# Performance work log

Measured on AMD Instinct MI355X. Metric: run time of the kernel, lower is better.

## Reference

```python
import jax, jax.numpy as jnp
import numpy as np


def setup_inputs() -> dict:
    key = jax.random.key(0)
    ks = jax.random.split(key, 8)
    T, B, D = 2048, 8, 1024
    d, NM, k = 64, 8, 2
    Mp1 = NM + 1
    s_in = 1.0 / np.sqrt(D)
    X = jax.random.normal(ks[0], (T, B, D), dtype=jnp.float32)
    M0 = 0.02 * jax.random.normal(ks[1], (d, d), dtype=jnp.float32)
    W_q = s_in * jax.random.normal(ks[2], (D, d), dtype=jnp.float32)
    b_q = jnp.zeros((d,), jnp.float32)
    W_k = s_in * jax.random.normal(ks[3], (D, Mp1 * d), dtype=jnp.float32)
    b_k = jnp.zeros((Mp1 * d,), jnp.float32)
    W_v = s_in * jax.random.normal(ks[4], (D, Mp1 * d), dtype=jnp.float32)
    b_v = jnp.zeros((Mp1 * d,), jnp.float32)
    W_g = s_in * jax.random.normal(ks[5], (D, NM), dtype=jnp.float32)
    b_g = jnp.zeros((NM,), jnp.float32)
    return dict(X=X, M0=M0, W_q=W_q, b_q=b_q, W_k=W_k, b_k=b_k,
                W_v=W_v, b_v=b_v, W_g=W_g, b_g=b_g, k=k)


def _mom_forward(X, M0, W_q, b_q, W_k, b_k, W_v, b_v, W_g, b_g, k):
    T, B, D = X.shape
    d = M0.shape[0]
    NM = W_g.shape[1]
    Mp1 = NM + 1  # memory 0 is the always-on shared memory
    Kp1 = k + 1
    # --- gating + top-k memory selection ---
    scores = jax.nn.softmax(X @ W_g + b_g, axis=-1)               # (T,B,NM)
    m_sc, m_idx = jax.lax.top_k(scores, k)                        # (T,B,k)
    m_sc = m_sc / jnp.sum(m_sc, axis=-1, keepdims=True)
    m_idx = m_idx + 1                                             # shift: 0 reserved for shared memory
    idx_u = jnp.concatenate([jnp.zeros((T, B, 1), m_idx.dtype), m_idx], axis=2)  # (T,B,Kp1)
    sc_u = jnp.concatenate([jnp.ones((T, B, 1), m_sc.dtype), m_sc], axis=2)      # (T,B,Kp1)
    # --- varlen pack: sort replicated tokens by (batch, memory, time) ---
    # NB: the torch build_varlen_pack runs under @torch.no_grad -> detached
    t_rep = jnp.broadcast_to(jnp.arange(T)[:, None, None], (T, B, Kp1)).reshape(-1)
    b_rep = jnp.broadcast_to(jnp.arange(B)[None, :, None], (T, B, Kp1)).reshape(-1)
    m_rep = idx_u.reshape(-1)
    sort_key = b_rep * (Mp1 * T) + m_rep * T + t_rep              # unique per packed token
    perm = jnp.argsort(sort_key)
    t_o = t_rep[perm]
    b_o = b_rep[perm]
    m_id = m_rep[perm]
    alpha = jax.lax.stop_gradient(sc_u.reshape(-1)[perm])         # (Tt,)
    x_tilde = jax.lax.stop_gradient(
        jnp.broadcast_to(X[:, :, None, :], (T, B, Kp1, D)).reshape(-1, D)[perm])  # (Tt,D)
    Tt = T * B * Kp1
    # segment id per packed token; state resets at each new (batch, memory) segment
    seg = b_o * Mp1 + m_id
    new_seg = jnp.concatenate([jnp.ones((1,), bool), seg[1:] != seg[:-1]])
    # --- projections; pick k/v head matching each token's routed memory ---
    q_t = x_tilde @ W_q + b_q                                     # (Tt,d)
    K_all = (x_tilde @ W_k + b_k).reshape(Tt, Mp1, d)
    V_all = (x_tilde @ W_v + b_v).reshape(Tt, Mp1, d)
    k_t = jnp.take_along_axis(K_all, m_id[:, None, None], axis=1)[:, 0]  # (Tt,d)
    v_t = jnp.take_along_axis(V_all, m_id[:, None, None], axis=1)[:, 0]  # (Tt,d)
    # --- per-segment linear-attention recurrence: M_t = M0 + sum k_tau v_tau^T, o_t = q_t @ M_t ---
    def step(M, inp):
        qt, kt, vt, ns = inp
        M = jnp.where(ns, M0, M)
        M = M + kt[:, None] * vt[None, :]
        return M, qt @ M
    _, o_tilde = jax.lax.scan(step, M0, (q_t, k_t, v_t, new_seg))  # (Tt,d)
    # --- weighted scatter-add back to (T,B,d) ---
    o = jnp.zeros((T, B, d), X.dtype).at[t_o, b_o].add(alpha[:, None] * o_tilde)
    return o


def reference(X, M0, W_q, b_q, W_k, b_k, W_v, b_v, W_g, b_g, k):
    return _mom_forward(X, M0, W_q, b_q, W_k, b_k, W_v, b_v, W_g, b_g, k)
```

## Files before the change

kernel.cpp:

```cpp
#include <hip/hip_runtime.h>

#define TT   2048
#define BB   8
#define DD   1024
#define HD   64
#define MP1  9
#define NTOK (TT*BB)
#define CH   64
#define NC   32
#define NSEG (BB*MP1)
#define SEGCAP 2048
#define NCAT 1280
#define LDP  72
#define NZB  1024

typedef __attribute__((ext_vector_type(8))) short bf16x8;
typedef __attribute__((ext_vector_type(4))) float f32x4;

union U8 { uint4 v; unsigned short s[8]; };

static __device__ __forceinline__ unsigned short f2bf(float f) {
  union { float f; unsigned u; } c; c.f = f;
  unsigned r = (c.u + 0x7FFF + ((c.u >> 16) & 1)) >> 16;
  return (unsigned short)r;
}
static __device__ __forceinline__ float bf2f(unsigned short s) {
  union { unsigned u; float f; } c; c.u = ((unsigned)s) << 16;
  return c.f;
}

static __device__ __forceinline__ int sched_walk(
    const int* __restrict__ seglen, int bid, int* chunk_out) {
  const int batch = bid & 7;
  int idx = bid >> 3;
  for (int m = 0; m < MP1; m++) {
    int nch = (seglen[batch * MP1 + m] + 63) >> 6;
    if (idx < nch) { *chunk_out = idx; return batch * MP1 + m; }
    idx -= nch;
  }
  return -1;
}

__global__ __launch_bounds__(256) void prep(
    const float* __restrict__ X,
    const float* __restrict__ Wq, const float* __restrict__ Wk,
    const float* __restrict__ Wv, const float* __restrict__ bq,
    const float* __restrict__ bk, const float* __restrict__ bv,
    const float* __restrict__ Wg, const float* __restrict__ bg,
    unsigned short* __restrict__ Wt, float* __restrict__ bcat,
    int2* __restrict__ idxb, float2* __restrict__ alfb,
    unsigned short* __restrict__ Xb,
    float4* __restrict__ outz, int n4) {
  __shared__ float smem[8 * DD];
  const int tid = threadIdx.x;
  const int id = blockIdx.x;
  if (id >= 1344) {
    int i = (id - 1344) * 256 + tid;
    if (i < n4) outz[i] = make_float4(0.f, 0.f, 0.f, 0.f);
    return;
  }
  if (id < 320) {
    float (*tile)[65] = (float(*)[65])smem;
    const int n0 = (id % 20) * 64, k0 = (id / 20) * 64;
    const int c = tid & 63, rr = tid >> 6;
#pragma unroll 4
    for (int i = 0; i < 16; i++) {
      int kk = k0 + rr * 16 + i;
      int n  = n0 + c;
      float v = 0.f;
      if (n0 < 64)        v = Wq[kk * 64 + n];
      else if (n0 < 640)  v = Wk[kk * 576 + (n - 64)];
      else if (n0 < 1216) v = Wv[kk * 576 + (n - 640)];
      tile[rr * 16 + i][c] = v;
    }
    __syncthreads();
    const int lk = (tid & 15) * 4, ln = tid >> 4;
#pragma unroll
    for (int p = 0; p < 4; p++) {
      int nl = p * 16 + ln;
      ushort4 o;
      o.x = f2bf(tile[lk + 0][nl]); o.y = f2bf(tile[lk + 1][nl]);
      o.z = f2bf(tile[lk + 2][nl]); o.w = f2bf(tile[lk + 3][nl]);
      *(ushort4*)&Wt[(size_t)(n0 + nl) * DD + k0 + lk] = o;
    }
    if (id == 0) {
      for (int idx = tid; idx < NCAT; idx += 256) {
        float b = 0.f;
        if (idx < 64)        b = bq[idx];
        else if (idx < 640)  b = bk[idx - 64];
        else if (idx < 1216) b = bv[idx - 640];
        bcat[idx] = b;
      }
    }
    return;
  }
  float* wgT = smem;
#pragma unroll
  for (int idx4 = tid; idx4 < 2048; idx4 += 256) {
    float4 v = *(const float4*)&Wg[(size_t)idx4 * 4];
    int flat = idx4 * 4;
    int i = flat >> 3, j = flat & 7;
    wgT[(j + 0) * DD + i] = v.x;
    wgT[(j + 1) * DD + i] = v.y;
    wgT[(j + 2) * DD + i] = v.z;
    wgT[(j + 3) * DD + i] = v.w;
  }
  __syncthreads();
  const int lane = tid & 63, wave = tid >> 6;
  const int base_tok = (id - 320) * 16 + wave * 4;
  for (int tk = 0; tk < 4; tk++) {
    const int tok = base_tok + tk;
    const float* xr = X + (size_t)tok * DD;
    unsigned short* xbr = Xb + ((size_t)((tok & 7) * TT + (tok >> 3))) * DD;
    float p[8] = {0.f,0.f,0.f,0.f,0.f,0.f,0.f,0.f};
#pragma unroll
    for (int it = 0; it < 4; it++) {
      int i = it * 256 + lane * 4;
      float4 x = *(const float4*)&xr[i];
      ushort4 o;
      o.x = f2bf(x.x); o.y = f2bf(x.y); o.z = f2bf(x.z); o.w = f2bf(x.w);
      *(ushort4*)&xbr[i] = o;
#pragma unroll
      for (int j = 0; j < 8; j++) {
        float4 wv = *(const float4*)&wgT[j * DD + i];
        p[j] += x.x * wv.x + x.y * wv.y + x.z * wv.z + x.w * wv.w;
      }
    }
#pragma unroll
    for (int j = 0; j < 8; j++) {
      float v = p[j];
#pragma unroll
      for (int off = 32; off > 0; off >>= 1) v += __shfl_xor(v, off);
      p[j] = v + bg[j];
    }
    if (lane == 0) {
      int i1 = 0; float z1 = p[0];
#pragma unroll
      for (int j = 1; j < 8; j++) if (p[j] > z1) { z1 = p[j]; i1 = j; }
      int i2 = -1; float z2 = -3.0e38f;
#pragma unroll
      for (int j = 0; j < 8; j++) if (j != i1 && p[j] > z2) { z2 = p[j]; i2 = j; }
      float e   = expf(z2 - z1);
      float inv = 1.0f / (1.0f + e);
      idxb[tok] = make_int2(i1 + 1, i2 + 1);
      alfb[tok] = make_float2(inv, e * inv);
    }
  }
}

__global__ __launch_bounds__(1024) void pack_kernel(
    const int2* __restrict__ idxb, const float2* __restrict__ alfb,
    int* __restrict__ tlist, float* __restrict__ alist,
    int* __restrict__ seglen) {
  const int seg = blockIdx.x;
  const int b = seg / MP1, m = seg % MP1;
  const int tid = threadIdx.x;
  int* tl = tlist + (size_t)seg * SEGCAP;
  float* al = alist + (size_t)seg * SEGCAP;
  if (m == 0) {
    for (int pos = tid; pos < TT; pos += 1024) { tl[pos] = pos; al[pos] = 1.f; }
    if (tid == 0) seglen[seg] = TT;
    return;
  }
  __shared__ int wsum[16];
  const int lane = tid & 63, w = tid >> 6;
  int base = 0;
  for (int r = 0; r < TT / 1024; r++) {
    int t = r * 1024 + tid;
    int2 ix = idxb[t * BB + b];
    bool f = (ix.x == m || ix.y == m);
    float2 af = alfb[t * BB + b];
    float alpha = (ix.x == m) ? af.x : af.y;
    unsigned long long mask = __ballot(f);
    int lanepos = __popcll(mask & ((1ull << lane) - 1ull));
    if (lane == 0) wsum[w] = __popcll(mask);
    __syncthreads();
    int wbase = 0, total = 0;
#pragma unroll
    for (int i = 0; i < 16; i++) { int v = wsum[i]; if (i < w) wbase += v; total += v; }
    if (f) { int pos = base + wbase + lanepos; tl[pos] = t; al[pos] = alpha; }
    base += total;
    __syncthreads();
  }
  if (tid == 0) seglen[seg] = base;
  int Lpad = (base + 63) & ~63;
  for (int pos = base + tid; pos < Lpad; pos += 1024) { tl[pos] = 0; al[pos] = 0.f; }
}

#define ABUF_H 2048
#define BBUF_H 6144

__global__ __launch_bounds__(256) void pkv_intra(
    const unsigned short* __restrict__ Xb, const unsigned short* __restrict__ Wt,
    const float* __restrict__ bcat,
    const int* __restrict__ tlist, const float* __restrict__ alist,
    const int* __restrict__ seglen,
    unsigned short* __restrict__ Sb16, unsigned short* __restrict__ Qd,
    float* __restrict__ out) {
  int chunk;
  const int seg = sched_walk(seglen, blockIdx.x, &chunk);
  if (seg < 0) return;
  const int t0 = chunk * 64;
  const int L = seglen[seg];
  const int b = seg / MP1, m = seg % MP1;
  __shared__ unsigned short lds[4 * 64 * LDP];
  __shared__ int tls[64];
  unsigned short* Asb = lds;
  unsigned short* Bsb = lds + 2 * ABUF_H;
  const int tid = threadIdx.x;
  const int lane = tid & 63, w = tid >> 6;
  if (tid < 64) tls[tid] = tlist[(size_t)seg * SEGCAP + t0 + tid];
  __syncthreads();

  const int lrow = lane >> 2;
  const int lk   = (lane & 3) * 8;
  const unsigned short* aPtr = Xb + ((size_t)b * TT + tls[w * 16 + lrow]) * DD + lk;
  const unsigned short* kPtr = Wt + (size_t)(64  + m * 64 + w * 16 + lrow) * DD + lk;
  const unsigned short* vPtr = Wt + (size_t)(640 + m * 64 + w * 16 + lrow) * DD + lk;
  const unsigned short* qPtr = Wt + (size_t)(w * 16 + lrow) * DD + lk;

  const int wr = (w >> 1) * 32;
  const int wc64 = (w & 1);
  const int quad = lane >> 4, l15 = lane & 15;

  float biasv[4], qbias[2];
#pragma unroll
  for (int n = 0; n < 4; n++) {
    int col = wc64 * 64 + n * 16 + l15;
    biasv[n] = bcat[col < 64 ? (64 + m * 64 + col) : (640 + m * 64 + (col - 64))];
  }
#pragma unroll
  for (int i = 0; i < 2; i++) qbias[i] = bcat[wc64 * 32 + i * 16 + l15];
  asm volatile("s_waitcnt vmcnt(0)" ::: "memory");
  __builtin_amdgcn_sched_barrier(0);

  f32x4 acc[2][4];
  f32x4 qacc[2][2];
#pragma unroll
  for (int i = 0; i < 2; i++) {
#pragma unroll
    for (int j = 0; j < 4; j++) acc[i][j] = (f32x4){0.f, 0.f, 0.f, 0.f};
#pragma unroll
    for (int j = 0; j < 2; j++) qacc[i][j] = (f32x4){0.f, 0.f, 0.f, 0.f};
  }

#define STG(BUF, K0)                                                             \
  do {                                                                           \
    unsigned short* As_ = Asb + (BUF) * ABUF_H;                                  \
    unsigned short* Bs_ = Bsb + (BUF) * BBUF_H;                                  \
    __builtin_amdgcn_global_load_lds(                                            \
        (const __attribute__((address_space(1))) unsigned int*)(aPtr + (K0)),    \
        (__attribute__((address_space(3))) unsigned int*)(As_ + w * 512),        \
        16, 0, 0);                                                               \
    __builtin_amdgcn_global_load_lds(                                            \
        (const __attribute__((address_space(1))) unsigned int*)(kPtr + (K0)),    \
        (__attribute__((address_space(3))) unsigned int*)(Bs_ + w * 512),        \
        16, 0, 0);                                                               \
    __builtin_amdgcn_global_load_lds(                                            \
        (const __attribute__((address_space(1))) unsigned int*)(vPtr + (K0)),    \
        (__attribute__((address_space(3))) unsigned int*)(Bs_ + 2048 + w * 512), \
        16, 0, 0);                                                               \
    __builtin_amdgcn_global_load_lds(                                            \
        (const __attribute__((address_space(1))) unsigned int*)(qPtr + (K0)),    \
        (__attribute__((address_space(3))) unsigned int*)(Bs_ + 4096 + w * 512), \
        16, 0, 0);                                                               \
  } while (0)

#define CMP(BUF)                                                                 \
  do {                                                                           \
    const unsigned short* As_ = Asb + (BUF) * ABUF_H;                            \
    const unsigned short* Bs_ = Bsb + (BUF) * BBUF_H;                            \
    bf16x8 af[2], bfr[4];                                                        \
    _Pragma("unroll")                                                            \
    for (int i = 0; i < 2; i++)                                                  \
      af[i] = *(const bf16x8*)&As_[(wr + i * 16 + l15) * 32 + quad * 8];         \
    _Pragma("unroll")                                                            \
    for (int n = 0; n < 4; n++)                                                  \
      bfr[n] = *(const bf16x8*)&Bs_[wc64 * 2048 + (n * 16 + l15) * 32 + quad * 8]; \
    _Pragma("unroll")                                                            \
    for (int mi = 0; mi < 2; mi++)                                               \
      _Pragma("unroll")                                                          \
      for (int ni = 0; ni < 4; ni++)                                             \
        acc[mi][ni] = __builtin_amdgcn_mfma_f32_16x16x32_bf16(af[mi], bfr[ni], acc[mi][ni], 0, 0, 0); \
    {                                                                            \
      bf16x8 qf[2];                                                              \
      _Pragma("unroll")                                                          \
      for (int i = 0; i < 2; i++)                                                \
        qf[i] = *(const bf16x8*)&Bs_[4096 + (wc64 * 32 + i * 16 + l15) * 32 + quad * 8]; \
      _Pragma("unroll")                                                          \
      for (int mi = 0; mi < 2; mi++)                                             \
        _Pragma("unroll")                                                        \
        for (int ni = 0; ni < 2; ni++)                                           \
          qacc[mi][ni] = __builtin_amdgcn_mfma_f32_16x16x32_bf16(af[mi], qf[ni], qacc[mi][ni], 0, 0, 0); \
    }                                                                            \
  } while (0)

  STG(0, 0);
  STG(1, 32);
  for (int it = 0; it < 31; it++) {
    asm volatile("s_waitcnt vmcnt(4)" ::: "memory");
    __builtin_amdgcn_sched_barrier(0);
    asm volatile("s_barrier" ::: "memory");
    CMP(it & 1);
    asm volatile("s_waitcnt lgkmcnt(0)" ::: "memory");
    __builtin_amdgcn_sched_barrier(0);
    asm volatile("s_barrier" ::: "memory");
    if (it < 30) STG(it & 1, (it + 2) * 32);
  }
  asm volatile("s_waitcnt vmcnt(0)" ::: "memory");
  __builtin_amdgcn_sched_barrier(0);
  asm volatile("s_barrier" ::: "memory");
  CMP(1);
#undef STG
#undef CMP

  asm volatile("s_waitcnt lgkmcnt(0)" ::: "memory");
  __builtin_amdgcn_sched_barrier(0);
  __syncthreads();

  unsigned short* Qs  = lds;
  unsigned short* Ks  = lds + 64 * LDP;
  unsigned short* KTs = lds + 2 * 64 * LDP;
  unsigned short* VTs = lds + 3 * 64 * LDP;

#pragma unroll
  for (int ni = 0; ni < 2; ni++) {
    int qcol = wc64 * 32 + ni * 16 + l15;
#pragma unroll
    for (int mi = 0; mi < 2; mi++) {
#pragma unroll
      for (int r = 0; r < 4; r++) {
        int pr = wr + mi * 16 + quad * 4 + r;
        unsigned short qv = f2bf(qacc[mi][ni][r] + qbias[ni]);
        Qs[pr * LDP + qcol] = qv;
        if (m == 0) Qd[(size_t)((t0 + pr) * BB + b) * HD + qcol] = qv;
      }
    }
  }
#pragma unroll
  for (int ni = 0; ni < 4; ni++) {
    int col = ni * 16 + l15;
#pragma unroll
    for (int mi = 0; mi < 2; mi++) {
#pragma unroll
      for (int r = 0; r < 4; r++) {
        int pr = wr + mi * 16 + quad * 4 + r;
        unsigned short v = f2bf(acc[mi][ni][r] + biasv[ni]);
        if (wc64 == 0) {
          unsigned short kv = (t0 + pr < L) ? v : (unsigned short)0;
          Ks[pr * LDP + col]  = kv;
          KTs[col * LDP + pr] = kv;
        } else {
          VTs[col * LDP + pr] = v;
        }
      }
    }
  }
  __syncthreads();

  const int* tl = tlist + (size_t)seg * SEGCAP;
  {
    const unsigned short* arow = &VTs[(w * 16 + l15) * LDP];
    bf16x8 a0 = *(const bf16x8*)(arow + quad * 8);
    bf16x8 a1 = *(const bf16x8*)(arow + 32 + quad * 8);
    unsigned short* Sp = Sb16 + ((size_t)seg * NC + chunk) * 4096;
#pragma unroll
    for (int n = 0; n < 4; n++) {
      const unsigned short* brow = &KTs[(n * 16 + l15) * LDP];
      f32x4 a2 = __builtin_amdgcn_mfma_f32_16x16x32_bf16(a0, *(const bf16x8*)(brow + quad * 8),
                                                         (f32x4){0.f,0.f,0.f,0.f}, 0, 0, 0);
      a2 = __builtin_amdgcn_mfma_f32_16x16x32_bf16(a1, *(const bf16x8*)(brow + 32 + quad * 8),
                                                   a2, 0, 0, 0);
#pragma unroll
      for (int r = 0; r < 4; r++)
        Sp[(w * 16 + quad * 4 + r) * 64 + n * 16 + l15] = f2bf(a2[r]);
    }
  }
  unsigned short* qrow = &Qs[(w * 16 + l15) * LDP];
  bf16x8 aq0 = *(const bf16x8*)(qrow + quad * 8);
  bf16x8 aq1 = *(const bf16x8*)(qrow + 32 + quad * 8);
  f32x4 pp[4];
#pragma unroll
  for (int n = 0; n < 4; n++) {
    const unsigned short* krow = &Ks[(n * 16 + l15) * LDP];
    pp[n] = __builtin_amdgcn_mfma_f32_16x16x32_bf16(aq0, *(const bf16x8*)(krow + quad * 8),
                                                    (f32x4){0.f,0.f,0.f,0.f}, 0, 0, 0);
    pp[n] = __builtin_amdgcn_mfma_f32_16x16x32_bf16(aq1, *(const bf16x8*)(krow + 32 + quad * 8),
                                                    pp[n], 0, 0, 0);
  }
#pragma unroll
  for (int n = 0; n < 4; n++)
#pragma unroll
    for (int r = 0; r < 4; r++) {
      int i = w * 16 + quad * 4 + r, j = n * 16 + l15;
      Qs[i * LDP + j] = (j <= i) ? f2bf(pp[n][r]) : (unsigned short)0;
    }
  bf16x8 ap0 = *(const bf16x8*)(qrow + quad * 8);
  bf16x8 ap1 = *(const bf16x8*)(qrow + 32 + quad * 8);
  f32x4 po[4];
#pragma unroll
  for (int n = 0; n < 4; n++) {
    const unsigned short* vrow = &VTs[(n * 16 + l15) * LDP];
    po[n] = __builtin_amdgcn_mfma_f32_16x16x32_bf16(ap0, *(const bf16x8*)(vrow + quad * 8),
                                                    (f32x4){0.f,0.f,0.f,0.f}, 0, 0, 0);
    po[n] = __builtin_amdgcn_mfma_f32_16x16x32_bf16(ap1, *(const bf16x8*)(vrow + 32 + quad * 8),
                                                    po[n], 0, 0, 0);
  }
#pragma unroll
  for (int r = 0; r < 4; r++) {
    int pos = t0 + w * 16 + quad * 4 + r;
    if (pos < L) {
      int t = tl[pos];
      float alpha = alist[(size_t)seg * SEGCAP + pos];
#pragma unroll
      for (int n = 0; n < 4; n++)
        atomicAdd(&out[(size_t)(t * BB + b) * HD + n * 16 + l15], alpha * po[n][r]);
    }
  }
}

__global__ __launch_bounds__(256) void scan_kernel(
    const float* __restrict__ M0, const int* __restrict__ seglen,
    unsigned short* __restrict__ Sb16) {
  const int batch = blockIdx.x & 7;
  const int idx = blockIdx.x >> 3;
  const int seg = batch * MP1 + (idx >> 2), slab = idx & 3;
  const int nch = (seglen[seg] + CH - 1) / CH;
  if (nch <= 0) return;
  const int tid = threadIdx.x;
  const int off = slab * 1024 + tid * 4;
  float run[4];
#pragma unroll
  for (int u = 0; u < 4; u++) {
    int o = off + u;
    run[u] = M0[(o & 63) * 64 + (o >> 6)];
  }
  unsigned short* base = Sb16 + (size_t)seg * NC * 4096;
  ushort4 s = *(const ushort4*)(base + off);
  for (int c = 0; c < nch; c++) {
    unsigned short* p = base + c * 4096 + off;
    ushort4 snext;
    if (c + 1 < nch) snext = *(const ushort4*)(p + 4096);
    ushort4 o;
    o.x = f2bf(run[0]); o.y = f2bf(run[1]); o.z = f2bf(run[2]); o.w = f2bf(run[3]);
    *(ushort4*)p = o;
    run[0] += bf2f(s.x); run[1] += bf2f(s.y); run[2] += bf2f(s.z); run[3] += bf2f(s.w);
    s = snext;
  }
}

__global__ __launch_bounds__(256) void chunk_inter(
    const unsigned short* __restrict__ Qd, const unsigned short* __restrict__ Sb16,
    const int* __restrict__ tlist, const float* __restrict__ alist,
    const int* __restrict__ seglen, float* __restrict__ out) {
  int chunk;
  const int seg = sched_walk(seglen, blockIdx.x, &chunk);
  if (seg < 0) return;
  const int L = seglen[seg];
  const int t0 = chunk * CH;
  __shared__ unsigned short Qs[64 * LDP];
  __shared__ unsigned short MT[64 * LDP];
  const int b = seg / MP1;
  const int tid = threadIdx.x;
  const int* tl = tlist + (size_t)seg * SEGCAP;
  {
    int row = tid >> 2, c16 = (tid & 3) << 4;
    int pos = t0 + row;
    const unsigned short* qb = Qd + (size_t)(tl[pos] * BB + b) * HD;
    *(uint4*)&Qs[row * LDP + c16]     = *(const uint4*)(qb + c16);
    *(uint4*)&Qs[row * LDP + c16 + 8] = *(const uint4*)(qb + c16 + 8);
    const unsigned short* Mp = Sb16 + ((size_t)seg * NC + chunk) * 4096 + row * 64 + c16;
    *(uint4*)&MT[row * LDP + c16]     = *(const uint4*)(Mp);
    *(uint4*)&MT[row * LDP + c16 + 8] = *(const uint4*)(Mp + 8);
  }
  __syncthreads();
  const int lane = tid & 63, w = tid >> 6;
  const int quad = lane >> 4, l15 = lane & 15;
  const unsigned short* qrow = &Qs[(w * 16 + l15) * LDP];
  bf16x8 aq0 = *(const bf16x8*)(qrow + quad * 8);
  bf16x8 aq1 = *(const bf16x8*)(qrow + 32 + quad * 8);
  f32x4 po[4];
#pragma unroll
  for (int n = 0; n < 4; n++) {
    const unsigned short* mrow = &MT[(n * 16 + l15) * LDP];
    po[n] = __builtin_amdgcn_mfma_f32_16x16x32_bf16(aq0, *(const bf16x8*)(mrow + quad * 8),
                                                    (f32x4){0.f,0.f,0.f,0.f}, 0, 0, 0);
    po[n] = __builtin_amdgcn_mfma_f32_16x16x32_bf16(aq1, *(const bf16x8*)(mrow + 32 + quad * 8),
                                                    po[n], 0, 0, 0);
  }
#pragma unroll
  for (int r = 0; r < 4; r++) {
    int pos = t0 + w * 16 + quad * 4 + r;
    if (pos < L) {
      int t = tl[pos];
      float alpha = alist[(size_t)seg * SEGCAP + pos];
#pragma unroll
      for (int n = 0; n < 4; n++)
        atomicAdd(&out[(size_t)(t * BB + b) * HD + n * 16 + l15], alpha * po[n][r]);
    }
  }
}

extern "C" void kernel_launch(void* const* d_in, const int* in_sizes, int n_in,
                              void* d_out, int out_size, void* d_ws, size_t ws_size,
                              hipStream_t stream) {
  const float* X  = (const float*)d_in[0];
  const float* M0 = (const float*)d_in[1];
  const float* Wq = (const float*)d_in[2];
  const float* bq = (const float*)d_in[3];
  const float* Wk = (const float*)d_in[4];
  const float* bk = (const float*)d_in[5];
  const float* Wv = (const float*)d_in[6];
  const float* bv = (const float*)d_in[7];
  const float* Wg = (const float*)d_in[8];
  const float* bg = (const float*)d_in[9];

  char* ws = (char*)d_ws;
  unsigned short* Xb   = (unsigned short*)(ws);
  unsigned short* Wt   = (unsigned short*)(ws + 33554432ULL);
  float*          bcat = (float*)         (ws + 36175872ULL);
  unsigned short* Qd   = (unsigned short*)(ws + 36180992ULL);
  unsigned short* Sb16 = (unsigned short*)(ws + 76026880ULL);
  int2*           idxb = (int2*)          (ws + 94901248ULL);
  float2*         alfb = (float2*)        (ws + 95032320ULL);
  int*            tlist= (int*)           (ws + 95163392ULL);
  float*          alist= (float*)         (ws + 95753216ULL);
  int*            slen = (int*)           (ws + 96343040ULL);

  float* out = (float*)d_out;
  const int n4 = out_size / 4;

  prep<<<320 + NTOK / 16 + NZB, 256, 0, stream>>>(
      X, Wq, Wk, Wv, bq, bk, bv, Wg, bg, Wt, bcat, idxb, alfb, Xb,
      (float4*)out, n4);
  pack_kernel<<<NSEG, 1024, 0, stream>>>(idxb, alfb, tlist, alist, slen);
  pkv_intra<<<1024, 256, 0, stream>>>(Xb, Wt, bcat, tlist, alist, slen, Sb16, Qd, out);
  scan_kernel<<<288, 256, 0, stream>>>(M0, slen, Sb16);
  chunk_inter<<<1024, 256, 0, stream>>>(Qd, Sb16, tlist, alist, slen, out);
}
```

Measured before the change: 120.1 us.

## Load GEMM operands directly from global into registers, dropping LDS staging

Replaces the double-buffered global_load_lds staging and barrier-synchronised LDS reads in the projection GEMM with direct per-lane 16-byte global loads feeding the MFMA fragments. It also adds a minimum-blocks-per-CU hint to launch_bounds. The aim is to remove LDS round trips and block-wide barriers in the K loop and raise occupancy. The cost is that operands shared between waves are loaded redundantly from global or L2, and memory latency is no longer hidden by explicit prefetching.

```diff
diff --git a/kernel.cpp b/kernel.cpp
--- a/kernel.cpp
+++ b/kernel.cpp
@@ -187,10 +187,7 @@
   for (int pos = base + tid; pos < Lpad; pos += 1024) { tl[pos] = 0; al[pos] = 0.f; }
 }
 
-#define ABUF_H 2048
-#define BBUF_H 6144
-
-__global__ __launch_bounds__(256) void pkv_intra(
+__global__ __launch_bounds__(256, 3) void pkv_intra(
     const unsigned short* __restrict__ Xb, const unsigned short* __restrict__ Wt,
     const float* __restrict__ bcat,
     const int* __restrict__ tlist, const float* __restrict__ alist,
@@ -205,20 +202,11 @@
   const int b = seg / MP1, m = seg % MP1;
   __shared__ unsigned short lds[4 * 64 * LDP];
   __shared__ int tls[64];
-  unsigned short* Asb = lds;
-  unsigned short* Bsb = lds + 2 * ABUF_H;
   const int tid = threadIdx.x;
   const int lane = tid & 63, w = tid >> 6;
   if (tid < 64) tls[tid] = tlist[(size_t)seg * SEGCAP + t0 + tid];
   __syncthreads();
 
-  const int lrow = lane >> 2;
-  const int lk   = (lane & 3) * 8;
-  const unsigned short* aPtr = Xb + ((size_t)b * TT + tls[w * 16 + lrow]) * DD + lk;
-  const unsigned short* kPtr = Wt + (size_t)(64  + m * 64 + w * 16 + lrow) * DD + lk;
-  const unsigned short* vPtr = Wt + (size_t)(640 + m * 64 + w * 16 + lrow) * DD + lk;
-  const unsigned short* qPtr = Wt + (size_t)(w * 16 + lrow) * DD + lk;
-
   const int wr = (w >> 1) * 32;
   const int wc64 = (w & 1);
   const int quad = lane >> 4, l15 = lane & 15;
@@ -231,8 +219,16 @@
   }
 #pragma unroll
   for (int i = 0; i < 2; i++) qbias[i] = bcat[wc64 * 32 + i * 16 + l15];
-  asm volatile("s_waitcnt vmcnt(0)" ::: "memory");
-  __builtin_amdgcn_sched_barrier(0);
+
+  const unsigned short* aP0 = Xb + ((size_t)b * TT + tls[wr + l15]) * DD + quad * 8;
+  const unsigned short* aP1 = Xb + ((size_t)b * TT + tls[wr + 16 + l15]) * DD + quad * 8;
+  const int bsec = (wc64 ? 640 : 64) + m * 64;
+  const unsigned short* bP0 = Wt + (size_t)(bsec + 0  + l15) * DD + quad * 8;
+  const unsigned short* bP1 = Wt + (size_t)(bsec + 16 + l15) * DD + quad * 8;
+  const unsigned short* bP2 = Wt + (size_t)(bsec + 32 + l15) * DD + quad * 8;
+  const unsigned short* bP3 = Wt + (size_t)(bsec + 48 + l15) * DD + quad * 8;
+  const unsigned short* qP0 = Wt + (size_t)(wc64 * 32 + l15) * DD + quad * 8;
+  const unsigned short* qP1 = Wt + (size_t)(wc64 * 32 + 16 + l15) * DD + quad * 8;
 
   f32x4 acc[2][4];
   f32x4 qacc[2][2];
@@ -244,79 +240,30 @@
     for (int j = 0; j < 2; j++) qacc[i][j] = (f32x4){0.f, 0.f, 0.f, 0.f};
   }
 
-#define STG(BUF, K0)                                                             \
-  do {                                                                           \
-    unsigned short* As_ = Asb + (BUF) * ABUF_H;                                  \
-    unsigned short* Bs_ = Bsb + (BUF) * BBUF_H;                                  \
-    __builtin_amdgcn_global_load_lds(                                            \
-        (const __attribute__((address_space(1))) unsigned int*)(aPtr + (K0)),    \
-        (__attribute__((address_space(3))) unsigned int*)(As_ + w * 512),        \
-        16, 0, 0);                                                               \
-    __builtin_amdgcn_global_load_lds(                                            \
-        (const __attribute__((address_space(1))) unsigned int*)(kPtr + (K0)),    \
-        (__attribute__((address_space(3))) unsigned int*)(Bs_ + w * 512),        \
-        16, 0, 0);                                                               \
-    __builtin_amdgcn_global_load_lds(                                            \
-        (const __attribute__((address_space(1))) unsigned int*)(vPtr + (K0)),    \
-        (__attribute__((address_space(3))) unsigned int*)(Bs_ + 2048 + w * 512), \
-        16, 0, 0);                                                               \
-    __builtin_amdgcn_global_load_lds(                                            \
-        (const __attribute__((address_space(1))) unsigned int*)(qPtr + (K0)),    \
-        (__attribute__((address_space(3))) unsigned int*)(Bs_ + 4096 + w * 512), \
-        16, 0, 0);                                                               \
-  } while (0)
-
-#define CMP(BUF)                                                                 \
-  do {                                                                           \
-    const unsigned short* As_ = Asb + (BUF) * ABUF_H;                            \
-    const unsigned short* Bs_ = Bsb + (BUF) * BBUF_H;                            \
-    bf16x8 af[2], bfr[4];                                                        \
-    _Pragma("unroll")                                                            \
-    for (int i = 0; i < 2; i++)                                                  \
-      af[i] = *(const bf16x8*)&As_[(wr + i * 16 + l15) * 32 + quad * 8];         \
-    _Pragma("unroll")                                                            \
-    for (int n = 0; n < 4; n++)                                                  \
-      bfr[n] = *(const bf16x8*)&Bs_[wc64 * 2048 + (n * 16 + l15) * 32 + quad * 8]; \
-    _Pragma("unroll")                                                            \
-    for (int mi = 0; mi < 2; mi++)                                               \
-      _Pragma("unroll")                                                          \
-      for (int ni = 0; ni < 4; ni++)                                             \
-        acc[mi][ni] = __builtin_amdgcn_mfma_f32_16x16x32_bf16(af[mi], bfr[ni], acc[mi][ni], 0, 0, 0); \
-    {                                                                            \
-      bf16x8 qf[2];                                                              \
-      _Pragma("unroll")                                                          \
-      for (int i = 0; i < 2; i++)                                                \
-        qf[i] = *(const bf16x8*)&Bs_[4096 + (wc64 * 32 + i * 16 + l15) * 32 + quad * 8]; \
-      _Pragma("unroll")                                                          \
-      for (int mi = 0; mi < 2; mi++)                                             \
-        _Pragma("unroll")                                                        \
-        for (int ni = 0; ni < 2; ni++)                                           \
-          qacc[mi][ni] = __builtin_amdgcn_mfma_f32_16x16x32_bf16(af[mi], qf[ni], qacc[mi][ni], 0, 0, 0); \
-    }                                                                            \
-  } while (0)
-
-  STG(0, 0);
-  STG(1, 32);
-  for (int it = 0; it < 31; it++) {
-    asm volatile("s_waitcnt vmcnt(4)" ::: "memory");
-    __builtin_amdgcn_sched_barrier(0);
-    asm volatile("s_barrier" ::: "memory");
-    CMP(it & 1);
-    asm volatile("s_waitcnt lgkmcnt(0)" ::: "memory");
-    __builtin_amdgcn_sched_barrier(0);
-    asm volatile("s_barrier" ::: "memory");
-    if (it < 30) STG(it & 1, (it + 2) * 32);
-  }
-  asm volatile("s_waitcnt vmcnt(0)" ::: "memory");
-  __builtin_amdgcn_sched_barrier(0);
-  asm volatile("s_barrier" ::: "memory");
-  CMP(1);
-#undef STG
-#undef CMP
-
-  asm volatile("s_waitcnt lgkmcnt(0)" ::: "memory");
-  __builtin_amdgcn_sched_barrier(0);
-  __syncthreads();
+#pragma unroll 2
+  for (int kk = 0; kk < 32; kk++) {
+    const int o = kk * 32;
+    bf16x8 af0 = *(const bf16x8*)(aP0 + o);
+    bf16x8 af1 = *(const bf16x8*)(aP1 + o);
+    bf16x8 b0  = *(const bf16x8*)(bP0 + o);
+    bf16x8 b1  = *(const bf16x8*)(bP1 + o);
+    bf16x8 b2  = *(const bf16x8*)(bP2 + o);
+    bf16x8 b3  = *(const bf16x8*)(bP3 + o);
+    bf16x8 q0  = *(const bf16x8*)(qP0 + o);
+    bf16x8 q1  = *(const bf16x8*)(qP1 + o);
+    acc[0][0] = __builtin_amdgcn_mfma_f32_16x16x32_bf16(af0, b0, acc[0][0], 0, 0, 0);
+    acc[0][1] = __builtin_amdgcn_mfma_f32_16x16x32_bf16(af0, b1, acc[0][1], 0, 0, 0);
+    acc[0][2] = __builtin_amdgcn_mfma_f32_16x16x32_bf16(af0, b2, acc[0][2], 0, 0, 0);
+    acc[0][3] = __builtin_amdgcn_mfma_f32_16x16x32_bf16(af0, b3, acc[0][3], 0, 0, 0);
+    acc[1][0] = __builtin_amdgcn_mfma_f32_16x16x32_bf16(af1, b0, acc[1][0], 0, 0, 0);
+    acc[1][1] = __builtin_amdgcn_mfma_f32_16x16x32_bf16(af1, b1, acc[1][1], 0, 0, 0);
+    acc[1][2] = __builtin_amdgcn_mfma_f32_16x16x32_bf16(af1, b2, acc[1][2], 0, 0, 0);
+    acc[1][3] = __builtin_amdgcn_mfma_f32_16x16x32_bf16(af1, b3, acc[1][3], 0, 0, 0);
+    qacc[0][0] = __builtin_amdgcn_mfma_f32_16x16x32_bf16(af0, q0, qacc[0][0], 0, 0, 0);
+    qacc[0][1] = __builtin_amdgcn_mfma_f32_16x16x32_bf16(af0, q1, qacc[0][1], 0, 0, 0);
+    qacc[1][0] = __builtin_amdgcn_mfma_f32_16x16x32_bf16(af1, q0, qacc[1][0], 0, 0, 0);
+    qacc[1][1] = __builtin_amdgcn_mfma_f32_16x16x32_bf16(af1, q1, qacc[1][1], 0, 0, 0);
+  }
 
   unsigned short* Qs  = lds;
   unsigned short* Ks  = lds + 64 * LDP;
```

New measurement: 181.8 us. 51.4% more time.
